# Optimization experiments

Measured on AMD Instinct MI355X. Metric: run time of the kernel, lower is better.

The kernel has to match this reference:

```python
import jax, jax.numpy as jnp
import numpy as np

S = 14          # grid size
B = 2           # boxes per cell
NCLS = 20       # number of classes
L_COORD = 5.0
L_NOOBJ = 0.5


def setup_inputs() -> dict:
    key = jax.random.key(0)
    k1, k2, k3, k4 = jax.random.split(key, 4)
    N = 4096
    pred_tensor = jax.random.uniform(k1, (N, S, S, B * 5 + NCLS), dtype=jnp.float32)
    target_boxes = jax.random.uniform(k2, (N, S, S, 4), dtype=jnp.float32)
    target_cls = jax.random.uniform(k3, (N, S, S, NCLS), dtype=jnp.float32)
    has_object_map = jax.random.randint(k4, (N, S, S), 0, 2) == 1
    return {
        "pred_tensor": pred_tensor,
        "target_boxes": target_boxes,
        "target_cls": target_cls,
        "has_object_map": has_object_map,
    }


def _yolo_loss(pred_tensor, target_boxes, target_cls, has_object_map):
    N = pred_tensor.shape[0]
    inv_n = 1.0 / N
    m = has_object_map.astype(pred_tensor.dtype)            # (N,S,S) 1 where object

    pred_boxes = pred_tensor[..., : B * 5].reshape(*pred_tensor.shape[:3], B, 5)  # (N,S,S,B,5)
    pred_cls = pred_tensor[..., B * 5:]                     # (N,S,S,20)

    # class loss over object cells (masked sum == boolean-index + sum)
    cls_loss = jnp.sum(m[..., None] * (pred_cls - target_cls) ** 2) * inv_n

    # no-object confidence loss: all B confidences at non-object cells vs 0
    conf = pred_boxes[..., 4]                               # (N,S,S,B)
    no_obj_loss = jnp.sum((1.0 - m)[..., None] * conf ** 2) * inv_n

    # per-cell IoU of each of the B predicted boxes against the target box.
    # xywh2xyxy: center x,y are divided by S; w,h used directly (as in source).
    xy = pred_boxes[..., :2] / S                            # (N,S,S,B,2)
    wh = pred_boxes[..., 2:4]                               # (N,S,S,B,2)
    p1 = xy - wh / 2
    p2 = xy + wh / 2
    t = target_boxes[..., None, :]                          # (N,S,S,1,4) treated as xyxy
    lt = jnp.maximum(p1, t[..., :2])
    rb = jnp.minimum(p2, t[..., 2:])
    iwh = jnp.clip(rb - lt, 0.0)
    inter = iwh[..., 0] * iwh[..., 1]                       # (N,S,S,B)
    area_p = wh[..., 0] * wh[..., 1]                        # (x2-x1)*(y2-y1) = w*h
    area_t = (t[..., 2] - t[..., 0]) * (t[..., 3] - t[..., 1])
    iou = inter / (area_p + area_t - inter)                 # (N,S,S,B)

    # best-of-B selection per cell (torch.max picks first max index -> argmax)
    best_idx = jnp.argmax(iou, axis=-1)                     # (N,S,S)
    best_boxes = jnp.take_along_axis(
        pred_boxes, best_idx[..., None, None], axis=3
    )[..., 0, :]                                            # (N,S,S,5)

    # containing-object confidence loss: best conf vs 1.0 at object cells
    containing_obj_loss = jnp.sum(m * (best_boxes[..., 4] - 1.0) ** 2) * inv_n

    center_loss = jnp.sum(m[..., None] * (best_boxes[..., :2] - target_boxes[..., :2]) ** 2)
    dim_loss = jnp.sum(
        m[..., None]
        * (jnp.sqrt(best_boxes[..., 2:4]) - jnp.sqrt(target_boxes[..., 2:4])) ** 2
    )
    reg_loss = (center_loss + dim_loss) * inv_n

    total_loss = cls_loss + L_NOOBJ * no_obj_loss + L_COORD * reg_loss + containing_obj_loss
    # [total, reg, containing_obj, no_obj, cls]
    return jnp.stack([total_loss, reg_loss, containing_obj_loss, no_obj_loss, cls_loss])


def reference(pred_tensor, target_boxes, target_cls, has_object_map):
    return _yolo_loss(pred_tensor, target_boxes, target_cls, has_object_map)
```

## Files before the change

### kernel.cpp

```cpp
#include <hip/hip_runtime.h>


#define NCELLS (4096 * 14 * 14)
#define NBLOCKS (NCELLS / 256)


__global__ void yolo_zero_kernel(float* __restrict__ ws) {
    if (threadIdx.x < 16) ws[threadIdx.x] = 0.0f;
}

__global__ void yolo_detect_kernel(const unsigned char* __restrict__ mb,
                                   int* __restrict__ flag) {
    int t = threadIdx.x;
    unsigned int found = 0;
#pragma unroll
    for (int k = 0; k < 16; ++k) {
        int slot = t * 16 + k;
        found |= mb[4 * slot + 1] | mb[4 * slot + 2] | mb[4 * slot + 3];
    }
    if (found) atomicOr(flag, 1);
}

__global__ __launch_bounds__(256) void yolo_main_kernel(
    const float* __restrict__ pred,
    const float* __restrict__ tbox,
    const float* __restrict__ tcls,
    const void* __restrict__ mask,
    const int* __restrict__ flag,
    float* __restrict__ ws) {
    const int c = blockIdx.x * 256 + threadIdx.x;

    float pv[30];
    {
        const float2* p2 = (const float2*)(pred + (long long)30 * c);
#pragma unroll
        for (int k = 0; k < 15; ++k) {
            float2 t = p2[k];
            pv[2 * k] = t.x;
            pv[2 * k + 1] = t.y;
        }
    }
    const float4 tb = *(const float4*)(tbox + (long long)4 * c);
    float tc[20];
    {
        const float4* c4 = (const float4*)(tcls + (long long)20 * c);
#pragma unroll
        for (int k = 0; k < 5; ++k) {
            float4 t = c4[k];
            tc[4 * k] = t.x;
            tc[4 * k + 1] = t.y;
            tc[4 * k + 2] = t.z;
            tc[4 * k + 3] = t.w;
        }
    }
    const int mode = *flag;
    float m;
    if (mode) {
        m = ((const unsigned char*)mask)[c] ? 1.0f : 0.0f;
    } else {
        m = ((const int*)mask)[c] ? 1.0f : 0.0f;
    }

    float s = 0.0f;
#pragma unroll
    for (int i = 0; i < 20; ++i) {
        float d = pv[10 + i] - tc[i];
        s += d * d;
    }
    float cls_s = m * s;

    float conf0 = pv[4], conf1 = pv[9];
    float noobj_s = (1.0f - m) * (conf0 * conf0 + conf1 * conf1);

    float iou[2];
    float at = (tb.z - tb.x) * (tb.w - tb.y);
#pragma unroll
    for (int b = 0; b < 2; ++b) {
        int base = 5 * b;
        float x = pv[base] / 14.0f;
        float y = pv[base + 1] / 14.0f;
        float w = pv[base + 2];
        float h = pv[base + 3];
        float p1x = x - w * 0.5f, p1y = y - h * 0.5f;
        float p2x = x + w * 0.5f, p2y = y + h * 0.5f;
        float ltx = fmaxf(p1x, tb.x), lty = fmaxf(p1y, tb.y);
        float rbx = fminf(p2x, tb.z), rby = fminf(p2y, tb.w);
        float iw = fmaxf(rbx - ltx, 0.0f), ih = fmaxf(rby - lty, 0.0f);
        float inter = iw * ih;
        float ap = w * h;
        iou[b] = inter / (ap + at - inter);
    }
    int best = (iou[1] > iou[0]) ? 5 : 0;
    float bx = pv[best], by = pv[best + 1], bw = pv[best + 2], bh = pv[best + 3],
          bc = pv[best + 4];

    float contain_s = m * (bc - 1.0f) * (bc - 1.0f);

    float dx = bx - tb.x, dy = by - tb.y;
    float dw = sqrtf(bw) - sqrtf(tb.z);
    float dh = sqrtf(bh) - sqrtf(tb.w);
    float reg_s = m * (dx * dx + dy * dy + dw * dw + dh * dh);

#pragma unroll
    for (int off = 32; off > 0; off >>= 1) {
        cls_s += __shfl_down(cls_s, off, 64);
        noobj_s += __shfl_down(noobj_s, off, 64);
        contain_s += __shfl_down(contain_s, off, 64);
        reg_s += __shfl_down(reg_s, off, 64);
    }
    __shared__ float red[4][4];
    int lane = threadIdx.x & 63;
    int wid = threadIdx.x >> 6;
    if (lane == 0) {
        red[wid][0] = cls_s;
        red[wid][1] = noobj_s;
        red[wid][2] = contain_s;
        red[wid][3] = reg_s;
    }
    __syncthreads();
    if (threadIdx.x < 4) {
        float v = red[0][threadIdx.x] + red[1][threadIdx.x] +
                  red[2][threadIdx.x] + red[3][threadIdx.x];
        atomicAdd(&ws[threadIdx.x], v);
    }
}

__global__ void yolo_final_kernel(const float* __restrict__ ws,
                                  float* __restrict__ out) {
    if (threadIdx.x == 0) {
        const float inv_n = 1.0f / 4096.0f;
        float cls = ws[0] * inv_n;
        float noobj = ws[1] * inv_n;
        float contain = ws[2] * inv_n;
        float reg = ws[3] * inv_n;
        float total = cls + 0.5f * noobj + 5.0f * reg + contain;
        out[0] = total;
        out[1] = reg;
        out[2] = contain;
        out[3] = noobj;
        out[4] = cls;
    }
}

extern "C" void kernel_launch(void* const* d_in, const int* in_sizes, int n_in,
                              void* d_out, int out_size, void* d_ws,
                              size_t ws_size, hipStream_t stream) {
    const float* pred = (const float*)d_in[0];
    const float* tbox = (const float*)d_in[1];
    const float* tcls = (const float*)d_in[2];
    const void* mask = d_in[3];
    float* ws = (float*)d_ws;
    float* out = (float*)d_out;

    yolo_zero_kernel<<<1, 64, 0, stream>>>(ws);
    yolo_detect_kernel<<<1, 256, 0, stream>>>((const unsigned char*)mask,
                                              (int*)(ws + 8));
    yolo_main_kernel<<<NBLOCKS, 256, 0, stream>>>(pred, tbox, tcls, mask,
                                                  (const int*)(ws + 8), ws);
    yolo_final_kernel<<<1, 64, 0, stream>>>(ws, out);
}
```

Measured before the change: 207.2 us.

## Fuse detect/final into main kernel and stage pred/cls loads through LDS

Loads of pred and target_cls now go through shared memory. Each block reads its contiguous chunk with coalesced float4 loads and stores it into a padded LDS layout, then each thread reads its own cell from there. This replaces the earlier strided per-thread float2/float4 loads. The mask-format detection moves into each block via a ballot over the first 256 words, and a last-block-done atomic counter replaces the separate final kernel, so the launch count drops from four to two. The cost is about 53 KB of LDS per block, which limits occupancy, plus an extra barrier and a threadfence per block.

```diff
diff --git a/kernel.cpp b/kernel.cpp
--- a/kernel.cpp
+++ b/kernel.cpp
@@ -9,51 +9,70 @@
     if (threadIdx.x < 16) ws[threadIdx.x] = 0.0f;
 }
 
-__global__ void yolo_detect_kernel(const unsigned char* __restrict__ mb,
-                                   int* __restrict__ flag) {
-    int t = threadIdx.x;
-    unsigned int found = 0;
-#pragma unroll
-    for (int k = 0; k < 16; ++k) {
-        int slot = t * 16 + k;
-        found |= mb[4 * slot + 1] | mb[4 * slot + 2] | mb[4 * slot + 3];
-    }
-    if (found) atomicOr(flag, 1);
-}
-
-__global__ __launch_bounds__(256) void yolo_main_kernel(
+__global__ __launch_bounds__(256) void yolo_fused_kernel(
     const float* __restrict__ pred,
     const float* __restrict__ tbox,
     const float* __restrict__ tcls,
     const void* __restrict__ mask,
-    const int* __restrict__ flag,
-    float* __restrict__ ws) {
-    const int c = blockIdx.x * 256 + threadIdx.x;
+    float* __restrict__ ws,
+    float* __restrict__ out) {
+    __shared__ float sp[256 * 31];
+    __shared__ float sc[256 * 21];
+    __shared__ float red[4][4];
+    __shared__ int ired[4];
 
-    float pv[30];
+    const int t = threadIdx.x;
+    const int lane = t & 63;
+    const int wid = t >> 6;
+    const int c0 = blockIdx.x << 8;
+    const int c = c0 + t;
+
     {
-        const float2* p2 = (const float2*)(pred + (long long)30 * c);
+        const unsigned int dv = ((const unsigned int*)mask)[t] & 0xFFFFFF00u;
+        const unsigned long long bal = __ballot(dv != 0u);
+        if (lane == 0) ired[wid] = (bal != 0ULL) ? 1 : 0;
+    }
+
+    const float4 tb = ((const float4*)tbox)[c];
+
+    {
+        const float4* p4 = (const float4*)(pred + (long long)c0 * 30);
 #pragma unroll
-        for (int k = 0; k < 15; ++k) {
-            float2 t = p2[k];
-            pv[2 * k] = t.x;
-            pv[2 * k + 1] = t.y;
+        for (int i = 0; i < 8; ++i) {
+            const int g = t + 256 * i;
+            if (g < 1920) {
+                const float4 v = p4[g];
+                const int j = 4 * g;
+                const int q = j / 30;
+                const int r = j - 30 * q;
+                const int a = 31 * q + r;
+                const int cr = (r == 28);
+                sp[a] = v.x;
+                sp[a + 1] = v.y;
+                sp[a + 2 + cr] = v.z;
+                sp[a + 3 + cr] = v.w;
+            }
         }
     }
-    const float4 tb = *(const float4*)(tbox + (long long)4 * c);
-    float tc[20];
+
     {
-        const float4* c4 = (const float4*)(tcls + (long long)20 * c);
+        const float4* c4 = (const float4*)(tcls + (long long)c0 * 20);
 #pragma unroll
-        for (int k = 0; k < 5; ++k) {
-            float4 t = c4[k];
-            tc[4 * k] = t.x;
-            tc[4 * k + 1] = t.y;
-            tc[4 * k + 2] = t.z;
-            tc[4 * k + 3] = t.w;
+        for (int i = 0; i < 5; ++i) {
+            const int g = t + 256 * i;
+            const float4 v = c4[g];
+            const int q = g / 5;
+            const int a = 21 * q + 4 * (g - 5 * q);
+            sc[a] = v.x;
+            sc[a + 1] = v.y;
+            sc[a + 2] = v.z;
+            sc[a + 3] = v.w;
         }
     }
-    const int mode = *flag;
+
+    __syncthreads();
+
+    const int mode = ired[0] | ired[1] | ired[2] | ired[3];
     float m;
     if (mode) {
         m = ((const unsigned char*)mask)[c] ? 1.0f : 0.0f;
@@ -61,44 +80,51 @@
         m = ((const int*)mask)[c] ? 1.0f : 0.0f;
     }
 
+    const float* pc = sp + 31 * t;
+    const float* cc = sc + 21 * t;
+
     float s = 0.0f;
 #pragma unroll
     for (int i = 0; i < 20; ++i) {
-        float d = pv[10 + i] - tc[i];
+        const float d = pc[10 + i] - cc[i];
         s += d * d;
     }
     float cls_s = m * s;
 
-    float conf0 = pv[4], conf1 = pv[9];
+    float pv[10];
+#pragma unroll
+    for (int i = 0; i < 10; ++i) pv[i] = pc[i];
+
+    const float conf0 = pv[4], conf1 = pv[9];
     float noobj_s = (1.0f - m) * (conf0 * conf0 + conf1 * conf1);
 
     float iou[2];
-    float at = (tb.z - tb.x) * (tb.w - tb.y);
+    const float at = (tb.z - tb.x) * (tb.w - tb.y);
 #pragma unroll
     for (int b = 0; b < 2; ++b) {
-        int base = 5 * b;
-        float x = pv[base] / 14.0f;
-        float y = pv[base + 1] / 14.0f;
-        float w = pv[base + 2];
-        float h = pv[base + 3];
-        float p1x = x - w * 0.5f, p1y = y - h * 0.5f;
-        float p2x = x + w * 0.5f, p2y = y + h * 0.5f;
-        float ltx = fmaxf(p1x, tb.x), lty = fmaxf(p1y, tb.y);
-        float rbx = fminf(p2x, tb.z), rby = fminf(p2y, tb.w);
-        float iw = fmaxf(rbx - ltx, 0.0f), ih = fmaxf(rby - lty, 0.0f);
-        float inter = iw * ih;
-        float ap = w * h;
+        const int base = 5 * b;
+        const float x = pv[base] / 14.0f;
+        const float y = pv[base + 1] / 14.0f;
+        const float w = pv[base + 2];
+        const float h = pv[base + 3];
+        const float p1x = x - w * 0.5f, p1y = y - h * 0.5f;
+        const float p2x = x + w * 0.5f, p2y = y + h * 0.5f;
+        const float ltx = fmaxf(p1x, tb.x), lty = fmaxf(p1y, tb.y);
+        const float rbx = fminf(p2x, tb.z), rby = fminf(p2y, tb.w);
+        const float iw = fmaxf(rbx - ltx, 0.0f), ih = fmaxf(rby - lty, 0.0f);
+        const float inter = iw * ih;
+        const float ap = w * h;
         iou[b] = inter / (ap + at - inter);
     }
-    int best = (iou[1] > iou[0]) ? 5 : 0;
-    float bx = pv[best], by = pv[best + 1], bw = pv[best + 2], bh = pv[best + 3],
-          bc = pv[best + 4];
+    const int best = (iou[1] > iou[0]) ? 5 : 0;
+    const float bx = pv[best], by = pv[best + 1], bw = pv[best + 2],
+                bh = pv[best + 3], bc = pv[best + 4];
 
     float contain_s = m * (bc - 1.0f) * (bc - 1.0f);
 
-    float dx = bx - tb.x, dy = by - tb.y;
-    float dw = sqrtf(bw) - sqrtf(tb.z);
-    float dh = sqrtf(bh) - sqrtf(tb.w);
+    const float dx = bx - tb.x, dy = by - tb.y;
+    const float dw = sqrtf(bw) - sqrtf(tb.z);
+    const float dh = sqrtf(bh) - sqrtf(tb.w);
     float reg_s = m * (dx * dx + dy * dy + dw * dw + dh * dh);
 
 #pragma unroll
@@ -108,9 +134,6 @@
         contain_s += __shfl_down(contain_s, off, 64);
         reg_s += __shfl_down(reg_s, off, 64);
     }
-    __shared__ float red[4][4];
-    int lane = threadIdx.x & 63;
-    int wid = threadIdx.x >> 6;
     if (lane == 0) {
         red[wid][0] = cls_s;
         red[wid][1] = noobj_s;
@@ -118,27 +141,26 @@
         red[wid][3] = reg_s;
     }
     __syncthreads();
-    if (threadIdx.x < 4) {
-        float v = red[0][threadIdx.x] + red[1][threadIdx.x] +
-                  red[2][threadIdx.x] + red[3][threadIdx.x];
-        atomicAdd(&ws[threadIdx.x], v);
+    if (t < 4) {
+        const float v = red[0][t] + red[1][t] + red[2][t] + red[3][t];
+        atomicAdd(&ws[t], v);
     }
-}
 
-__global__ void yolo_final_kernel(const float* __restrict__ ws,
-                                  float* __restrict__ out) {
-    if (threadIdx.x == 0) {
-        const float inv_n = 1.0f / 4096.0f;
-        float cls = ws[0] * inv_n;
-        float noobj = ws[1] * inv_n;
-        float contain = ws[2] * inv_n;
-        float reg = ws[3] * inv_n;
-        float total = cls + 0.5f * noobj + 5.0f * reg + contain;
-        out[0] = total;
-        out[1] = reg;
-        out[2] = contain;
-        out[3] = noobj;
-        out[4] = cls;
+    __threadfence();
+    if (t == 0) {
+        const int done = atomicAdd((int*)ws + 4, 1);
+        if (done == NBLOCKS - 1) {
+            const float inv_n = 1.0f / 4096.0f;
+            const float cls = atomicAdd(&ws[0], 0.0f) * inv_n;
+            const float noobj = atomicAdd(&ws[1], 0.0f) * inv_n;
+            const float contain = atomicAdd(&ws[2], 0.0f) * inv_n;
+            const float reg = atomicAdd(&ws[3], 0.0f) * inv_n;
+            out[0] = cls + 0.5f * noobj + 5.0f * reg + contain;
+            out[1] = reg;
+            out[2] = contain;
+            out[3] = noobj;
+            out[4] = cls;
+        }
     }
 }
 
@@ -153,9 +175,6 @@
     float* out = (float*)d_out;
 
     yolo_zero_kernel<<<1, 64, 0, stream>>>(ws);
-    yolo_detect_kernel<<<1, 256, 0, stream>>>((const unsigned char*)mask,
-                                              (int*)(ws + 8));
-    yolo_main_kernel<<<NBLOCKS, 256, 0, stream>>>(pred, tbox, tcls, mask,
-                                                  (const int*)(ws + 8), ws);
-    yolo_final_kernel<<<1, 64, 0, stream>>>(ws, out);
+    yolo_fused_kernel<<<NBLOCKS, 256, 0, stream>>>(pred, tbox, tcls, mask, ws,
+                                                   out);
 }
```

After: 424.0 us. 2.05x slower.
